# Kernel optimization log

Measured on AMD Instinct MI355X. Metric: run time of the kernel, lower is better.

The kernel has to match this reference:

```python
import jax, jax.numpy as jnp
import numpy as np

EPS_W = 1e-8   # weight reciprocal eps (matches torch code)
EPS_BN = 1e-5  # torch BatchNorm1d default eps


def _cdist(a, b):
    # a: [B,N,3], b: [B,M,3] -> [B,N,M] euclidean distances
    sq = (jnp.sum(a * a, -1)[:, :, None] + jnp.sum(b * b, -1)[:, None, :]
          - 2.0 * jnp.einsum('bnd,bmd->bnm', a, b))
    return jnp.sqrt(jnp.maximum(sq, 0.0))


def _bn_relu(x, gamma, beta):
    # x: [B,C,N]; training-mode batch norm over (B,N)
    mean = jnp.mean(x, axis=(0, 2), keepdims=True)
    var = jnp.mean((x - mean) ** 2, axis=(0, 2), keepdims=True)
    y = (x - mean) * jax.lax.rsqrt(var + EPS_BN)
    y = y * gamma[None, :, None] + beta[None, :, None]
    return jax.nn.relu(y)


def setup_inputs() -> dict:
    key = jax.random.key(0)
    ks = jax.random.split(key, 8)
    B, Np, Ns = 16, 1024, 4096
    Cp, Cs, Co = 256, 128, 256
    return {
        'xyz_prev': jax.random.normal(ks[0], (B, Np, 3), jnp.float32),
        'xyz_skip': jax.random.normal(ks[1], (B, Ns, 3), jnp.float32),
        'points_prev': jax.random.normal(ks[2], (B, Cp, Np), jnp.float32),
        'points_skip': jax.random.normal(ks[3], (B, Cs, Ns), jnp.float32),
        'W1': jax.random.normal(ks[4], (Co, Cp + Cs), jnp.float32) * 0.05,
        'g1': jnp.ones((Co,), jnp.float32),
        'b1': jnp.zeros((Co,), jnp.float32),
        'W2': jax.random.normal(ks[5], (Co, Co), jnp.float32) * 0.05,
        'g2': jnp.ones((Co,), jnp.float32),
        'b2': jnp.zeros((Co,), jnp.float32),
    }


def reference(xyz_prev, xyz_skip, points_prev, points_skip, W1, g1, b1, W2, g2, b2):
    dist = _cdist(xyz_skip, xyz_prev)                       # [B,Ns,Np]
    neg, idx = jax.lax.top_k(-dist, 3)                      # 3 smallest dists
    dist_recip = 1.0 / (dist + EPS_W)
    # NOTE: normalization is over ALL N_prev points (faithful to source)
    weight = dist_recip / jnp.sum(dist_recip, axis=2, keepdims=True)
    w3 = jnp.take_along_axis(weight, idx, axis=2)           # [B,Ns,3]
    pp = jnp.swapaxes(points_prev, 1, 2)                    # [B,Np,Cp]
    g = jnp.take_along_axis(pp[:, None, :, :], idx[..., None], axis=2)  # [B,Ns,3,Cp]
    interp = jnp.einsum('bnk,bnkc->bcn', w3, g)             # [B,Cp,Ns]
    x = jnp.concatenate([interp, points_skip], axis=1)      # [B,Cp+Cs,Ns]
    x = _bn_relu(jnp.einsum('bcn,oc->bon', x, W1), g1, b1)
    x = _bn_relu(jnp.einsum('bcn,oc->bon', x, W2), g2, b2)
    return x
```

## Files before the change

kernel.cpp:

```cpp
#include <hip/hip_runtime.h>
#include <math.h>

constexpr int NB  = 16;
constexpr int NP  = 1024;
constexpr int NS  = 4096;
constexpr int CP  = 256;
constexpr int CS  = 128;
constexpr int CIN = 384;
constexpr int CO  = 256;

constexpr int NCHUNK = 16;
constexpr int CHPTS  = NP / NCHUNK;

typedef unsigned int uint;
typedef unsigned short ushort_t;
typedef __attribute__((ext_vector_type(8))) short short8;
typedef __attribute__((ext_vector_type(4))) float f32x4;

__device__ __forceinline__ ushort_t f2bf(float f) {
  uint u = __float_as_uint(f);
  uint r = (u + 0x7fffu + ((u >> 16) & 1u)) >> 16;
  return (ushort_t)r;
}
__device__ __forceinline__ float bf2f(ushort_t u) {
  return __uint_as_float(((uint)u) << 16);
}
__device__ __forceinline__ uint pk2(ushort_t lo, ushort_t hi) {
  return (uint)lo | ((uint)hi << 16);
}

__device__ __forceinline__ void gload16(const void* g, void* l) {
  __builtin_amdgcn_global_load_lds(
      (const __attribute__((address_space(1))) uint*)g,
      (__attribute__((address_space(3))) uint*)l, 16, 0, 0);
}

__device__ __forceinline__ void tkp(float pxv, float pyv, float pzv, int pi,
                                    float qx, float qy, float qz,
                                    float& k0, float& k1, float& k2,
                                    float& rsum) {
  float dx = pxv - qx, dy = pyv - qy, dz = pzv - qz;
  float sq = fmaf(dz, dz, fmaf(dy, dy, fmaf(dx, dx, 1e-16f)));
  rsum += __builtin_amdgcn_rsqf(sq);
  float k = __uint_as_float((__float_as_uint(sq) & 0xFFFFFC00u) | (uint)pi);
  k2 = __builtin_amdgcn_fmed3f(k1, k2, k);
  k1 = __builtin_amdgcn_fmed3f(k0, k1, k);
  k0 = fminf(k0, k);
}

__global__ __launch_bounds__(256) void topk_chunk_kernel(
    const float* __restrict__ xyz_prev, const float* __restrict__ xyz_skip,
    float* __restrict__ pbuf) {
  __shared__ float px[CHPTS], py[CHPTS], pz[CHPTS];
  int q  = blockIdx.y;
  int b  = blockIdx.z;
  int tid = threadIdx.x;
  if (tid < CHPTS) {
    const float* xp = xyz_prev + ((size_t)b * NP + q * CHPTS + tid) * 3;
    px[tid] = xp[0]; py[tid] = xp[1]; pz[tid] = xp[2];
  }
  __syncthreads();
  int nA = blockIdx.x * 512 + tid;
  int nB = nA + 256;
  const float* xqA = xyz_skip + ((size_t)b * NS + nA) * 3;
  const float* xqB = xyz_skip + ((size_t)b * NS + nB) * 3;
  float qxA = xqA[0], qyA = xqA[1], qzA = xqA[2];
  float qxB = xqB[0], qyB = xqB[1], qzB = xqB[2];
  float kA0 = INFINITY, kA1 = INFINITY, kA2 = INFINITY;
  float kB0 = INFINITY, kB1 = INFINITY, kB2 = INFINITY;
  float rsA = 0.f, rsB = 0.f;
  int pbase = q * CHPTS;

  for (int p = 0; p < CHPTS; p += 4) {
    float4 X = *(const float4*)&px[p];
    float4 Y = *(const float4*)&py[p];
    float4 Z = *(const float4*)&pz[p];
    tkp(X.x, Y.x, Z.x, pbase + p + 0, qxA, qyA, qzA, kA0, kA1, kA2, rsA);
    tkp(X.x, Y.x, Z.x, pbase + p + 0, qxB, qyB, qzB, kB0, kB1, kB2, rsB);
    tkp(X.y, Y.y, Z.y, pbase + p + 1, qxA, qyA, qzA, kA0, kA1, kA2, rsA);
    tkp(X.y, Y.y, Z.y, pbase + p + 1, qxB, qyB, qzB, kB0, kB1, kB2, rsB);
    tkp(X.z, Y.z, Z.z, pbase + p + 2, qxA, qyA, qzA, kA0, kA1, kA2, rsA);
    tkp(X.z, Y.z, Z.z, pbase + p + 2, qxB, qyB, qzB, kB0, kB1, kB2, rsB);
    tkp(X.w, Y.w, Z.w, pbase + p + 3, qxA, qyA, qzA, kA0, kA1, kA2, rsA);
    tkp(X.w, Y.w, Z.w, pbase + p + 3, qxB, qyB, qzB, kB0, kB1, kB2, rsB);
  }

  size_t PA = ((size_t)(b * NCHUNK + q) * NS + nA) * 4;
  size_t PB = ((size_t)(b * NCHUNK + q) * NS + nB) * 4;
  *(float4*)(pbuf + PA) = make_float4(kA0, kA1, kA2, rsA);
  *(float4*)(pbuf + PB) = make_float4(kB0, kB1, kB2, rsB);
}

__global__ __launch_bounds__(256) void topk_merge_kernel(
    const float* __restrict__ pbuf, float* __restrict__ w3,
    int* __restrict__ idx3) {
  int gid = blockIdx.x * 256 + threadIdx.x;
  int b = gid >> 12;
  int n = gid & (NS - 1);
  float k0 = INFINITY, k1 = INFINITY, k2 = INFINITY;
  float rsum = 0.f;
  #pragma unroll 4
  for (int q = 0; q < NCHUNK; q++) {
    float4 v = *(const float4*)(pbuf + ((size_t)(b * NCHUNK + q) * NS + n) * 4);
    rsum += v.w;
    k2 = __builtin_amdgcn_fmed3f(k1, k2, v.x);
    k1 = __builtin_amdgcn_fmed3f(k0, k1, v.x);
    k0 = fminf(k0, v.x);
    k2 = __builtin_amdgcn_fmed3f(k1, k2, v.y);
    k1 = __builtin_amdgcn_fmed3f(k0, k1, v.y);
    k0 = fminf(k0, v.y);
    k2 = __builtin_amdgcn_fmed3f(k1, k2, v.z);
    k1 = __builtin_amdgcn_fmed3f(k0, k1, v.z);
    k0 = fminf(k0, v.z);
  }
  float inv = 1.0f / rsum;
  uint u0 = __float_as_uint(k0), u1 = __float_as_uint(k1), u2 = __float_as_uint(k2);
  float d0 = __uint_as_float(u0 & 0xFFFFFC00u);
  float d1 = __uint_as_float(u1 & 0xFFFFFC00u);
  float d2 = __uint_as_float(u2 & 0xFFFFFC00u);
  size_t base = (size_t)gid * 3;
  w3[base + 0] = __builtin_amdgcn_rsqf(d0) * inv;
  w3[base + 1] = __builtin_amdgcn_rsqf(d1) * inv;
  w3[base + 2] = __builtin_amdgcn_rsqf(d2) * inv;
  idx3[base + 0] = (int)(u0 & 1023u);
  idx3[base + 1] = (int)(u1 & 1023u);
  idx3[base + 2] = (int)(u2 & 1023u);
}

__global__ __launch_bounds__(256) void wcast_kernel(
    const float* __restrict__ W1, const float* __restrict__ W2,
    ushort_t* __restrict__ W1b, ushort_t* __restrict__ W2b,
    float* __restrict__ st1, float* __restrict__ st2) {
  int tid = threadIdx.x;
  if (blockIdx.x == 0) {
    st1[tid] = 0.f; st1[tid + 256] = 0.f;
    st2[tid] = 0.f; st2[tid + 256] = 0.f;
  }
  int t = blockIdx.x * 256 + tid;
  int n1 = CO * CIN / 4;
  if (t < n1) {
    float4 v = *(const float4*)(W1 + t * 4);
    ushort4 o; o.x = f2bf(v.x); o.y = f2bf(v.y); o.z = f2bf(v.z); o.w = f2bf(v.w);
    *(ushort4*)(W1b + t * 4) = o;
  } else {
    int u = t - n1;
    float4 v = *(const float4*)(W2 + u * 4);
    ushort4 o; o.x = f2bf(v.x); o.y = f2bf(v.y); o.z = f2bf(v.z); o.w = f2bf(v.w);
    *(ushort4*)(W2b + u * 4) = o;
  }
}

__global__ __launch_bounds__(256) void ppT_kernel(
    const float* __restrict__ pp, ushort_t* __restrict__ pptT) {
  __shared__ float tl[64][65];
  int p0 = blockIdx.x * 64, c0 = blockIdx.y * 64, b = blockIdx.z;
  int tid = threadIdx.x;
  const float* P = pp + (size_t)b * CP * NP;
  int pi4 = (tid & 15) * 4, ci = tid >> 4;
  #pragma unroll
  for (int r = 0; r < 4; r++) {
    int cc = ci + 16 * r;
    float4 v = *(const float4*)(P + (size_t)(c0 + cc) * NP + p0 + pi4);
    tl[cc][pi4] = v.x; tl[cc][pi4 + 1] = v.y; tl[cc][pi4 + 2] = v.z; tl[cc][pi4 + 3] = v.w;
  }
  __syncthreads();
  ushort_t* O = pptT + (size_t)b * NP * CP;
  int ci4 = (tid & 15) * 4, pi = tid >> 4;
  #pragma unroll
  for (int r = 0; r < 4; r++) {
    int pr = pi + 16 * r;
    ushort4 o;
    o.x = f2bf(tl[ci4 + 0][pr]); o.y = f2bf(tl[ci4 + 1][pr]);
    o.z = f2bf(tl[ci4 + 2][pr]); o.w = f2bf(tl[ci4 + 3][pr]);
    *(ushort4*)(O + (size_t)(p0 + pr) * CP + c0 + ci4) = o;
  }
}

__global__ __launch_bounds__(256) void skipT_kernel(
    const float* __restrict__ sk, ushort_t* __restrict__ x1) {
  __shared__ float tl[64][65];
  int n0 = blockIdx.x * 64, c0 = blockIdx.y * 64, b = blockIdx.z;
  int tid = threadIdx.x;
  const float* S = sk + (size_t)b * CS * NS;
  int ni4 = (tid & 15) * 4, ci = tid >> 4;
  #pragma unroll
  for (int r = 0; r < 4; r++) {
    int cc = ci + 16 * r;
    float4 v = *(const float4*)(S + (size_t)(c0 + cc) * NS + n0 + ni4);
    tl[cc][ni4] = v.x; tl[cc][ni4 + 1] = v.y; tl[cc][ni4 + 2] = v.z; tl[cc][ni4 + 3] = v.w;
  }
  __syncthreads();
  ushort_t* O = x1 + (size_t)b * NS * CIN;
  int ci4 = (tid & 15) * 4, ni = tid >> 4;
  #pragma unroll
  for (int r = 0; r < 4; r++) {
    int nr = ni + 16 * r;
    ushort4 o;
    o.x = f2bf(tl[ci4 + 0][nr]); o.y = f2bf(tl[ci4 + 1][nr]);
    o.z = f2bf(tl[ci4 + 2][nr]); o.w = f2bf(tl[ci4 + 3][nr]);
    *(ushort4*)(O + (size_t)(n0 + nr) * CIN + CP + c0 + ci4) = o;
  }
}

__global__ __launch_bounds__(256) void interp_kernel(
    const ushort_t* __restrict__ pptT, const float* __restrict__ w3,
    const int* __restrict__ idx3, ushort_t* __restrict__ x1) {
  int tid = threadIdx.x;
  int nl = tid >> 6, l = tid & 63;
  int b = blockIdx.y;
  int n = blockIdx.x * 4 + nl;
  size_t nb = (size_t)b * NS + n;
  int j0 = idx3[nb * 3 + 0], j1 = idx3[nb * 3 + 1], j2 = idx3[nb * 3 + 2];
  float w0 = w3[nb * 3 + 0], w1 = w3[nb * 3 + 1], w2 = w3[nb * 3 + 2];
  const ushort_t* P = pptT + (size_t)b * NP * CP;
  int c = l * 4;
  ushort4 g0 = *(const ushort4*)(P + (size_t)j0 * CP + c);
  ushort4 g1 = *(const ushort4*)(P + (size_t)j1 * CP + c);
  ushort4 g2 = *(const ushort4*)(P + (size_t)j2 * CP + c);
  ushort4 o;
  o.x = f2bf(w0 * bf2f(g0.x) + w1 * bf2f(g1.x) + w2 * bf2f(g2.x));
  o.y = f2bf(w0 * bf2f(g0.y) + w1 * bf2f(g1.y) + w2 * bf2f(g2.y));
  o.z = f2bf(w0 * bf2f(g0.z) + w1 * bf2f(g1.z) + w2 * bf2f(g2.z));
  o.w = f2bf(w0 * bf2f(g0.w) + w1 * bf2f(g1.w) + w2 * bf2f(g2.w));
  *(ushort4*)(x1 + nb * CIN + c) = o;
}

template <int KD, bool ACT>
__global__ __launch_bounds__(256) void gemm_mfma_kernel(
    const ushort_t* __restrict__ X, const ushort_t* __restrict__ Wb,
    const float* __restrict__ stats_in, const float* __restrict__ g_in,
    const float* __restrict__ bt_in,
    ushort_t* __restrict__ Yb, float* __restrict__ stats) {
  __shared__ ushort_t ldsX[128 * 32];
  __shared__ ushort_t ldsW[128 * 32];
  __shared__ float ssum[128], ssq[128];
  __shared__ float a1s[ACT ? CO : 1], s1s[ACT ? CO : 1];
  int tid = threadIdx.x;
  int w = tid >> 6, l = tid & 63;
  int bid = blockIdx.x;
  int by = (bid >> 3) & 1;
  int s  = (bid & 7) + 8 * (bid >> 4);
  int bx = s & 31;
  int bz = s >> 5;
  int n0 = bx * 128;
  if (tid < 128) { ssum[tid] = 0.f; ssq[tid] = 0.f; }
  if constexpr (ACT) {
    float cnt = (float)NB * (float)NS;
    float m = stats_in[tid] / cnt;
    float var = stats_in[CO + tid] / cnt - m * m;
    var = fmaxf(var, 0.f);
    float invs = rsqrtf(var + 1e-5f);
    float av = g_in[tid] * invs;
    a1s[tid] = av; s1s[tid] = bt_in[tid] - m * av;
  }
  __syncthreads();

  f32x4 acc[4][4];
  #pragma unroll
  for (int i = 0; i < 4; i++)
    #pragma unroll
    for (int j = 0; j < 4; j++) acc[i][j] = {0.f, 0.f, 0.f, 0.f};

  int wn = (w & 1) * 64, wo = (w >> 1) * 64;
  int lr = l & 15, lk = l >> 4;
  const ushort_t* Xb = X + (size_t)bz * NS * KD;
  int rbase = w * 16 + (l >> 2);
  int cl = l & 3;
  int ksw = 8 * (cl ^ ((rbase >> 1) & 3));

  for (int kt = 0; kt < KD / 32; kt++) {
    int k0 = kt * 32;
    int ks = k0 + ksw;
    #pragma unroll
    for (int q = 0; q < 2; q++) {
      int r = q * 64 + rbase;
      gload16(Wb + (size_t)(by * 128 + r) * KD + ks, &ldsW[(q * 64 + w * 16) * 32]);
    }
    if constexpr (!ACT) {
      #pragma unroll
      for (int q = 0; q < 2; q++) {
        int r = q * 64 + rbase;
        gload16(Xb + (size_t)(n0 + r) * KD + ks, &ldsX[(q * 64 + w * 16) * 32]);
      }
    } else {
      float4 av0 = *(const float4*)&a1s[ks];
      float4 av1 = *(const float4*)&a1s[ks + 4];
      float4 sv0 = *(const float4*)&s1s[ks];
      float4 sv1 = *(const float4*)&s1s[ks + 4];
      #pragma unroll
      for (int q = 0; q < 2; q++) {
        int r = q * 64 + rbase;
        const ushort_t* src = Xb + (size_t)(n0 + r) * KD + ks;
        ushort4 v0 = *(const ushort4*)(src);
        ushort4 v1 = *(const ushort4*)(src + 4);
        int4 o;
        o.x = (int)pk2(f2bf(fmaxf(fmaf(av0.x, bf2f(v0.x), sv0.x), 0.f)),
                       f2bf(fmaxf(fmaf(av0.y, bf2f(v0.y), sv0.y), 0.f)));
        o.y = (int)pk2(f2bf(fmaxf(fmaf(av0.z, bf2f(v0.z), sv0.z), 0.f)),
                       f2bf(fmaxf(fmaf(av0.w, bf2f(v0.w), sv0.w), 0.f)));
        o.z = (int)pk2(f2bf(fmaxf(fmaf(av1.x, bf2f(v1.x), sv1.x), 0.f)),
                       f2bf(fmaxf(fmaf(av1.y, bf2f(v1.y), sv1.y), 0.f)));
        o.w = (int)pk2(f2bf(fmaxf(fmaf(av1.z, bf2f(v1.z), sv1.z), 0.f)),
                       f2bf(fmaxf(fmaf(av1.w, bf2f(v1.w), sv1.w), 0.f)));
        *(int4*)&ldsX[(q * 64 + w * 16) * 32 + l * 8] = o;
      }
    }
    __syncthreads();
    short8 a[4], bfr[4];
    #pragma unroll
    for (int i = 0; i < 4; i++) {
      int rr = wn + i * 16 + lr;
      int cs = lk ^ ((rr >> 1) & 3);
      a[i] = *(const short8*)&ldsX[rr * 32 + cs * 8];
    }
    #pragma unroll
    for (int j = 0; j < 4; j++) {
      int rr = wo + j * 16 + lr;
      int cs = lk ^ ((rr >> 1) & 3);
      bfr[j] = *(const short8*)&ldsW[rr * 32 + cs * 8];
    }
    #pragma unroll
    for (int i = 0; i < 4; i++)
      #pragma unroll
      for (int j = 0; j < 4; j++)
        acc[i][j] = __builtin_amdgcn_mfma_f32_16x16x32_bf16(a[i], bfr[j], acc[i][j], 0, 0, 0);
    __syncthreads();
  }

  #pragma unroll
  for (int j = 0; j < 4; j++) {
    int ol = wo + j * 16 + lr;
    int og = by * 128 + ol;
    float ps = 0.f, pq = 0.f;
    #pragma unroll
    for (int i = 0; i < 4; i++) {
      #pragma unroll
      for (int rg = 0; rg < 4; rg++) {
        float v = acc[i][j][rg];
        ps += v; pq += v * v;
        int n = n0 + wn + i * 16 + lk * 4 + rg;
        Yb[((size_t)bz * NS + n) * CO + og] = f2bf(v);
      }
    }
    atomicAdd(&ssum[ol], ps);
    atomicAdd(&ssq[ol], pq);
  }
  __syncthreads();
  if (tid < 128) {
    atomicAdd(&stats[by * 128 + tid], ssum[tid]);
    atomicAdd(&stats[CO + by * 128 + tid], ssq[tid]);
  }
}

__global__ __launch_bounds__(256) void bnrelu_tr_kernel(
    const ushort_t* __restrict__ y2b, const float* __restrict__ stats_in,
    const float* __restrict__ g_in, const float* __restrict__ bt_in,
    float* __restrict__ out) {
  __shared__ float tl[64][65];
  __shared__ float a2s[64], s2s[64];
  int n0 = blockIdx.x * 64, o0 = blockIdx.y * 64, b = blockIdx.z;
  const ushort_t* Y = y2b + (size_t)b * NS * CO;
  int tid = threadIdx.x;
  if (tid < 64) {
    int o = o0 + tid;
    float cnt = (float)NB * (float)NS;
    float m = stats_in[o] / cnt;
    float var = stats_in[CO + o] / cnt - m * m;
    var = fmaxf(var, 0.f);
    float invs = rsqrtf(var + 1e-5f);
    float av = g_in[o] * invs;
    a2s[tid] = av; s2s[tid] = bt_in[o] - m * av;
  }
  int o8 = (tid & 7) * 8, row = tid >> 3;
  #pragma unroll
  for (int r = 0; r < 2; r++) {
    int ii = row + 32 * r;
    const ushort_t* src = Y + (size_t)(n0 + ii) * CO + o0 + o8;
    ushort4 v0 = *(const ushort4*)(src);
    ushort4 v1 = *(const ushort4*)(src + 4);
    tl[ii][o8 + 0] = bf2f(v0.x); tl[ii][o8 + 1] = bf2f(v0.y);
    tl[ii][o8 + 2] = bf2f(v0.z); tl[ii][o8 + 3] = bf2f(v0.w);
    tl[ii][o8 + 4] = bf2f(v1.x); tl[ii][o8 + 5] = bf2f(v1.y);
    tl[ii][o8 + 6] = bf2f(v1.z); tl[ii][o8 + 7] = bf2f(v1.w);
  }
  __syncthreads();
  float* O = out + (size_t)b * CO * NS;
  int ii4 = (tid & 15) * 4, j = tid >> 4;
  #pragma unroll
  for (int r = 0; r < 4; r++) {
    int jj = j + 16 * r;
    float av = a2s[jj], sv = s2s[jj];
    float4 v;
    v.x = fmaxf(fmaf(av, tl[ii4 + 0][jj], sv), 0.f);
    v.y = fmaxf(fmaf(av, tl[ii4 + 1][jj], sv), 0.f);
    v.z = fmaxf(fmaf(av, tl[ii4 + 2][jj], sv), 0.f);
    v.w = fmaxf(fmaf(av, tl[ii4 + 3][jj], sv), 0.f);
    *(float4*)(O + (size_t)(o0 + jj) * NS + n0 + ii4) = v;
  }
}

extern "C" void kernel_launch(void* const* d_in, const int* in_sizes, int n_in,
                              void* d_out, int out_size, void* d_ws, size_t ws_size,
                              hipStream_t stream) {
  const float* xyz_prev    = (const float*)d_in[0];
  const float* xyz_skip    = (const float*)d_in[1];
  const float* points_prev = (const float*)d_in[2];
  const float* points_skip = (const float*)d_in[3];
  const float* W1 = (const float*)d_in[4];
  const float* g1 = (const float*)d_in[5];
  const float* b1 = (const float*)d_in[6];
  const float* W2 = (const float*)d_in[7];
  const float* g2 = (const float*)d_in[8];
  const float* b2 = (const float*)d_in[9];
  float* out = (float*)d_out;

  char* W = (char*)d_ws;
  size_t off = 0;
  auto alloc = [&](size_t bytes) {
    size_t o = off; off = (off + bytes + 255) & ~(size_t)255; return o;
  };
  ushort_t* x1   = (ushort_t*)(W + alloc((size_t)NB * NS * CIN * 2));
  ushort_t* y1b  = (ushort_t*)(W + alloc((size_t)NB * NS * CO * 2));
  ushort_t* pptT = (ushort_t*)(W + alloc((size_t)NB * NP * CP * 2));
  ushort_t* W1b  = (ushort_t*)(W + alloc((size_t)CO * CIN * 2));
  ushort_t* W2b  = (ushort_t*)(W + alloc((size_t)CO * CO * 2));
  float* w3   = (float*)(W + alloc((size_t)NB * NS * 3 * 4));
  int*   idx3 = (int*)(W + alloc((size_t)NB * NS * 3 * 4));
  float* st1  = (float*)(W + alloc(512 * 4));
  float* st2  = (float*)(W + alloc(512 * 4));
  size_t y2_off = alloc((size_t)NB * NS * CO * 2);
  bool full = (ws_size >= off);
  ushort_t* y2b = full ? (ushort_t*)(W + y2_off) : (ushort_t*)d_out;
  float* pbuf = full ? (float*)(W + y2_off) : (float*)d_out;

  hipLaunchKernelGGL(topk_chunk_kernel, dim3(NS / 512, NCHUNK, NB), dim3(256), 0,
                     stream, xyz_prev, xyz_skip, pbuf);
  hipLaunchKernelGGL(topk_merge_kernel, dim3(NB * NS / 256), dim3(256), 0, stream,
                     pbuf, w3, idx3);
  hipLaunchKernelGGL(wcast_kernel, dim3((CO * CIN / 4 + CO * CO / 4 + 255) / 256),
                     dim3(256), 0, stream, W1, W2, W1b, W2b, st1, st2);
  hipLaunchKernelGGL(ppT_kernel, dim3(NP / 64, CP / 64, NB), dim3(256), 0, stream,
                     points_prev, pptT);
  hipLaunchKernelGGL(skipT_kernel, dim3(NS / 64, CS / 64, NB), dim3(256), 0, stream,
                     points_skip, x1);
  hipLaunchKernelGGL(interp_kernel, dim3(NS / 4, NB), dim3(256), 0, stream,
                     pptT, w3, idx3, x1);
  hipLaunchKernelGGL((gemm_mfma_kernel<CIN, false>), dim3(1024), dim3(256),
                     0, stream, x1, W1b, (const float*)nullptr,
                     (const float*)nullptr, (const float*)nullptr, y1b, st1);
  hipLaunchKernelGGL((gemm_mfma_kernel<CO, true>), dim3(1024), dim3(256),
                     0, stream, y1b, W2b, st1, g1, b1, y2b, st2);
  if (full) {
    hipLaunchKernelGGL(bnrelu_tr_kernel, dim3(NS / 64, CO / 64, NB), dim3(256), 0,
                       stream, y2b, st2, g2, b2, out);
  } else {
    float* stage = (float*)d_ws;
    hipLaunchKernelGGL(bnrelu_tr_kernel, dim3(NS / 64, CO / 64, NB), dim3(256), 0,
                       stream, y2b, st2, g2, b2, stage);
    hipMemcpyAsync(out, stage, (size_t)NB * NS * CO * 4, hipMemcpyDeviceToDevice,
                   stream);
  }
}
```

Measured before the change: 157.9 us.

## Stage GEMM outputs through LDS, transpose in GEMM2, replicate BN stat atomics

GEMM epilogues now stage the bf16 tile in LDS and write it with 16-byte vector stores, replacing the scattered 2-byte stores of before. The second GEMM writes its output already transposed to channel-major, so the final BN+ReLU becomes a flat streaming kernel with no LDS transpose. BN statistics are spread over 8 replicated slots to reduce global atomic contention, and consumers sum the replicas. The larger LDS allocation may lower GEMM occupancy, and the strided LDS reads in the transposed epilogue could hit bank conflicts.

Result: slower. 166.5 us (+5.5%).

```diff
diff --git a/kernel.cpp b/kernel.cpp
--- a/kernel.cpp
+++ b/kernel.cpp
@@ -11,10 +11,12 @@
 
 constexpr int NCHUNK = 16;
 constexpr int CHPTS  = NP / NCHUNK;
+constexpr int NREP   = 8;
 
 typedef unsigned int uint;
 typedef unsigned short ushort_t;
 typedef __attribute__((ext_vector_type(8))) short short8;
+typedef __attribute__((ext_vector_type(8))) unsigned short us8;
 typedef __attribute__((ext_vector_type(4))) float f32x4;
 
 __device__ __forceinline__ ushort_t f2bf(float f) {
@@ -70,7 +72,6 @@
   float kB0 = INFINITY, kB1 = INFINITY, kB2 = INFINITY;
   float rsA = 0.f, rsB = 0.f;
   int pbase = q * CHPTS;
-
   for (int p = 0; p < CHPTS; p += 4) {
     float4 X = *(const float4*)&px[p];
     float4 Y = *(const float4*)&py[p];
@@ -84,7 +85,6 @@
     tkp(X.w, Y.w, Z.w, pbase + p + 3, qxA, qyA, qzA, kA0, kA1, kA2, rsA);
     tkp(X.w, Y.w, Z.w, pbase + p + 3, qxB, qyB, qzB, kB0, kB1, kB2, rsB);
   }
-
   size_t PA = ((size_t)(b * NCHUNK + q) * NS + nA) * 4;
   size_t PB = ((size_t)(b * NCHUNK + q) * NS + nB) * 4;
   *(float4*)(pbuf + PA) = make_float4(kA0, kA1, kA2, rsA);
@@ -132,9 +132,9 @@
     ushort_t* __restrict__ W1b, ushort_t* __restrict__ W2b,
     float* __restrict__ st1, float* __restrict__ st2) {
   int tid = threadIdx.x;
-  if (blockIdx.x == 0) {
-    st1[tid] = 0.f; st1[tid + 256] = 0.f;
-    st2[tid] = 0.f; st2[tid + 256] = 0.f;
+  if (blockIdx.x < 16) {
+    int i = blockIdx.x * 256 + tid;
+    st1[i] = 0.f; st2[i] = 0.f;
   }
   int t = blockIdx.x * 256 + tid;
   int n1 = CO * CIN / 4;
@@ -225,14 +225,15 @@
   *(ushort4*)(x1 + nb * CIN + c) = o;
 }
 
-template <int KD, bool ACT>
+template <int KD, bool ACT, bool TR_OUT>
 __global__ __launch_bounds__(256) void gemm_mfma_kernel(
     const ushort_t* __restrict__ X, const ushort_t* __restrict__ Wb,
     const float* __restrict__ stats_in, const float* __restrict__ g_in,
     const float* __restrict__ bt_in,
     ushort_t* __restrict__ Yb, float* __restrict__ stats) {
-  __shared__ ushort_t ldsX[128 * 32];
-  __shared__ ushort_t ldsW[128 * 32];
+  __shared__ __align__(16) char lds_raw[34048];
+  ushort_t* ldsX = (ushort_t*)lds_raw;
+  ushort_t* ldsW = (ushort_t*)(lds_raw + 8192);
   __shared__ float ssum[128], ssq[128];
   __shared__ float a1s[ACT ? CO : 1], s1s[ACT ? CO : 1];
   int tid = threadIdx.x;
@@ -245,10 +246,15 @@
   int n0 = bx * 128;
   if (tid < 128) { ssum[tid] = 0.f; ssq[tid] = 0.f; }
   if constexpr (ACT) {
+    float sm = 0.f, sq = 0.f;
+    #pragma unroll
+    for (int r = 0; r < NREP; r++) {
+      sm += stats_in[r * 512 + tid];
+      sq += stats_in[r * 512 + 256 + tid];
+    }
     float cnt = (float)NB * (float)NS;
-    float m = stats_in[tid] / cnt;
-    float var = stats_in[CO + tid] / cnt - m * m;
-    var = fmaxf(var, 0.f);
+    float m = sm / cnt;
+    float var = fmaxf(sq / cnt - m * m, 0.f);
     float invs = rsqrtf(var + 1e-5f);
     float av = g_in[tid] * invs;
     a1s[tid] = av; s1s[tid] = bt_in[tid] - m * av;
@@ -330,72 +336,92 @@
   #pragma unroll
   for (int j = 0; j < 4; j++) {
     int ol = wo + j * 16 + lr;
-    int og = by * 128 + ol;
     float ps = 0.f, pq = 0.f;
     #pragma unroll
-    for (int i = 0; i < 4; i++) {
-      #pragma unroll
-      for (int rg = 0; rg < 4; rg++) {
-        float v = acc[i][j][rg];
-        ps += v; pq += v * v;
-        int n = n0 + wn + i * 16 + lk * 4 + rg;
-        Yb[((size_t)bz * NS + n) * CO + og] = f2bf(v);
-      }
-    }
+    for (int i = 0; i < 4; i++)
+      #pragma unroll
+      for (int rg = 0; rg < 4; rg++) { float v = acc[i][j][rg]; ps += v; pq += v * v; }
     atomicAdd(&ssum[ol], ps);
     atomicAdd(&ssq[ol], pq);
   }
-  __syncthreads();
+  ushort_t* lout = (ushort_t*)lds_raw;
+  #pragma unroll
+  for (int i = 0; i < 4; i++)
+    #pragma unroll
+    for (int j = 0; j < 4; j++)
+      #pragma unroll
+      for (int rg = 0; rg < 4; rg++) {
+        int nl = wn + i * 16 + lk * 4 + rg;
+        int ol = wo + j * 16 + lr;
+        lout[nl * 132 + ol] = f2bf(acc[i][j][rg]);
+      }
+  __syncthreads();
+  if constexpr (!TR_OUT) {
+    int row = tid >> 1, half = tid & 1;
+    const ushort_t* src = lout + row * 132 + half * 64;
+    ushort_t* dst = Yb + ((size_t)bz * NS + n0 + row) * CO + by * 128 + half * 64;
+    #pragma unroll
+    for (int k = 0; k < 8; k++)
+      *(us8*)(dst + k * 8) = *(const us8*)(src + k * 8);
+  } else {
+    int ol = tid & 127, nh = tid >> 7;
+    us8 buf[8];
+    #pragma unroll
+    for (int k = 0; k < 8; k++) {
+      #pragma unroll
+      for (int e = 0; e < 8; e++)
+        buf[k][e] = lout[(nh * 64 + k * 8 + e) * 132 + ol];
+    }
+    ushort_t* dst = Yb + ((size_t)bz * CO + by * 128 + ol) * NS + n0 + nh * 64;
+    #pragma unroll
+    for (int k = 0; k < 8; k++)
+      *(us8*)(dst + k * 8) = buf[k];
+  }
   if (tid < 128) {
-    atomicAdd(&stats[by * 128 + tid], ssum[tid]);
-    atomicAdd(&stats[CO + by * 128 + tid], ssq[tid]);
-  }
-}
-
-__global__ __launch_bounds__(256) void bnrelu_tr_kernel(
-    const ushort_t* __restrict__ y2b, const float* __restrict__ stats_in,
+    int rep = bid & (NREP - 1);
+    atomicAdd(&stats[rep * 512 + by * 128 + tid], ssum[tid]);
+    atomicAdd(&stats[rep * 512 + 256 + by * 128 + tid], ssq[tid]);
+  }
+}
+
+__global__ __launch_bounds__(256) void bnrelu_lin_kernel(
+    const ushort_t* __restrict__ y2T, const float* __restrict__ stats_in,
     const float* __restrict__ g_in, const float* __restrict__ bt_in,
     float* __restrict__ out) {
-  __shared__ float tl[64][65];
-  __shared__ float a2s[64], s2s[64];
-  int n0 = blockIdx.x * 64, o0 = blockIdx.y * 64, b = blockIdx.z;
-  const ushort_t* Y = y2b + (size_t)b * NS * CO;
-  int tid = threadIdx.x;
-  if (tid < 64) {
-    int o = o0 + tid;
+  __shared__ float a2s[CO], s2s[CO];
+  int tid = threadIdx.x;
+  {
+    float sm = 0.f, sq = 0.f;
+    #pragma unroll
+    for (int r = 0; r < NREP; r++) {
+      sm += stats_in[r * 512 + tid];
+      sq += stats_in[r * 512 + 256 + tid];
+    }
     float cnt = (float)NB * (float)NS;
-    float m = stats_in[o] / cnt;
-    float var = stats_in[CO + o] / cnt - m * m;
-    var = fmaxf(var, 0.f);
+    float m = sm / cnt;
+    float var = fmaxf(sq / cnt - m * m, 0.f);
     float invs = rsqrtf(var + 1e-5f);
-    float av = g_in[o] * invs;
-    a2s[tid] = av; s2s[tid] = bt_in[o] - m * av;
-  }
-  int o8 = (tid & 7) * 8, row = tid >> 3;
-  #pragma unroll
-  for (int r = 0; r < 2; r++) {
-    int ii = row + 32 * r;
-    const ushort_t* src = Y + (size_t)(n0 + ii) * CO + o0 + o8;
-    ushort4 v0 = *(const ushort4*)(src);
-    ushort4 v1 = *(const ushort4*)(src + 4);
-    tl[ii][o8 + 0] = bf2f(v0.x); tl[ii][o8 + 1] = bf2f(v0.y);
-    tl[ii][o8 + 2] = bf2f(v0.z); tl[ii][o8 + 3] = bf2f(v0.w);
-    tl[ii][o8 + 4] = bf2f(v1.x); tl[ii][o8 + 5] = bf2f(v1.y);
-    tl[ii][o8 + 6] = bf2f(v1.z); tl[ii][o8 + 7] = bf2f(v1.w);
-  }
-  __syncthreads();
-  float* O = out + (size_t)b * CO * NS;
-  int ii4 = (tid & 15) * 4, j = tid >> 4;
-  #pragma unroll
-  for (int r = 0; r < 4; r++) {
-    int jj = j + 16 * r;
-    float av = a2s[jj], sv = s2s[jj];
-    float4 v;
-    v.x = fmaxf(fmaf(av, tl[ii4 + 0][jj], sv), 0.f);
-    v.y = fmaxf(fmaf(av, tl[ii4 + 1][jj], sv), 0.f);
-    v.z = fmaxf(fmaf(av, tl[ii4 + 2][jj], sv), 0.f);
-    v.w = fmaxf(fmaf(av, tl[ii4 + 3][jj], sv), 0.f);
-    *(float4*)(O + (size_t)(o0 + jj) * NS + n0 + ii4) = v;
+    float av = g_in[tid] * invs;
+    a2s[tid] = av; s2s[tid] = bt_in[tid] - m * av;
+  }
+  __syncthreads();
+  const size_t NV = (size_t)NB * CO * NS / 8;
+  for (size_t v = (size_t)blockIdx.x * 256 + tid; v < NV; v += 2048 * 256) {
+    size_t flat = v * 8;
+    int o = (int)((flat >> 12) & (CO - 1));
+    us8 x = *(const us8*)(y2T + flat);
+    float av = a2s[o], sv = s2s[o];
+    float4 r0, r1;
+    r0.x = fmaxf(fmaf(av, bf2f(x[0]), sv), 0.f);
+    r0.y = fmaxf(fmaf(av, bf2f(x[1]), sv), 0.f);
+    r0.z = fmaxf(fmaf(av, bf2f(x[2]), sv), 0.f);
+    r0.w = fmaxf(fmaf(av, bf2f(x[3]), sv), 0.f);
+    r1.x = fmaxf(fmaf(av, bf2f(x[4]), sv), 0.f);
+    r1.y = fmaxf(fmaf(av, bf2f(x[5]), sv), 0.f);
+    r1.z = fmaxf(fmaf(av, bf2f(x[6]), sv), 0.f);
+    r1.w = fmaxf(fmaf(av, bf2f(x[7]), sv), 0.f);
+    *(float4*)(out + flat) = r0;
+    *(float4*)(out + flat + 4) = r1;
   }
 }
 
@@ -426,8 +452,8 @@
   ushort_t* W2b  = (ushort_t*)(W + alloc((size_t)CO * CO * 2));
   float* w3   = (float*)(W + alloc((size_t)NB * NS * 3 * 4));
   int*   idx3 = (int*)(W + alloc((size_t)NB * NS * 3 * 4));
-  float* st1  = (float*)(W + alloc(512 * 4));
-  float* st2  = (float*)(W + alloc(512 * 4));
+  float* st1  = (float*)(W + alloc(NREP * 512 * 4));
+  float* st2  = (float*)(W + alloc(NREP * 512 * 4));
   size_t y2_off = alloc((size_t)NB * NS * CO * 2);
   bool full = (ws_size >= off);
   ushort_t* y2b = full ? (ushort_t*)(W + y2_off) : (ushort_t*)d_out;
@@ -445,18 +471,18 @@
                      points_skip, x1);
   hipLaunchKernelGGL(interp_kernel, dim3(NS / 4, NB), dim3(256), 0, stream,
                      pptT, w3, idx3, x1);
-  hipLaunchKernelGGL((gemm_mfma_kernel<CIN, false>), dim3(1024), dim3(256),
+  hipLaunchKernelGGL((gemm_mfma_kernel<CIN, false, false>), dim3(1024), dim3(256),
                      0, stream, x1, W1b, (const float*)nullptr,
                      (const float*)nullptr, (const float*)nullptr, y1b, st1);
-  hipLaunchKernelGGL((gemm_mfma_kernel<CO, true>), dim3(1024), dim3(256),
+  hipLaunchKernelGGL((gemm_mfma_kernel<CO, true, true>), dim3(1024), dim3(256),
                      0, stream, y1b, W2b, st1, g1, b1, y2b, st2);
   if (full) {
-    hipLaunchKernelGGL(bnrelu_tr_kernel, dim3(NS / 64, CO / 64, NB), dim3(256), 0,
-                       stream, y2b, st2, g2, b2, out);
+    hipLaunchKernelGGL(bnrelu_lin_kernel, dim3(2048), dim3(256), 0, stream,
+                       y2b, st2, g2, b2, out);
   } else {
     float* stage = (float*)d_ws;
-    hipLaunchKernelGGL(bnrelu_tr_kernel, dim3(NS / 64, CO / 64, NB), dim3(256), 0,
-                       stream, y2b, st2, g2, b2, stage);
+    hipLaunchKernelGGL(bnrelu_lin_kernel, dim3(2048), dim3(256), 0, stream,
+                       y2b, st2, g2, b2, stage);
     hipMemcpyAsync(out, stage, (size_t)NB * NS * CO * 4, hipMemcpyDeviceToDevice,
                    stream);
   }
```
